# Optimization experiments

Hardware: AMD Instinct MI355X
Metric: run time of the kernel (lower is better)

The kernel has to match this reference:

```python
import jax, jax.numpy as jnp
import numpy as np

EPS = 1e-7  # Keras K.epsilon()
ROUTINGS = 3

def squash(v, axis=-1):
    s2 = jnp.sum(jnp.square(v), axis=axis, keepdims=True)
    scale = s2 / (1.0 + s2) / jnp.sqrt(s2 + EPS)
    return scale * v

def setup_inputs() -> dict:
    key = jax.random.key(0)
    k1, k2 = jax.random.split(key)
    inputs = jax.random.normal(k1, (64, 1152, 8), dtype=jnp.float32)
    W = jax.random.normal(k2, (8, 43, 16), dtype=jnp.float32) * 0.1  # glorot-ish scale
    return {"inputs": inputs, "W": W}

def reference(inputs, W):
    # inputs: [b, i, j] (batch, input_num_capsule, input_dim_capsule)
    # W: [j, k, l] -> inputs_hat: [b, i, k, l]
    inputs_hat = jnp.einsum('bij,jkl->bikl', inputs, W)
    b_sz, I, N, _ = inputs_hat.shape
    b = jnp.zeros((b_sz, I, N), dtype=inputs_hat.dtype)
    outputs = None
    for r in range(ROUTINGS):
        c = jax.nn.softmax(b, axis=2)                       # [b, i, k]
        s = jnp.einsum('bik,bikl->bkl', c, inputs_hat)      # [b, k, l]
        outputs = squash(s, axis=-1)                         # [b, k, l]
        if r < ROUTINGS - 1:
            agreement = jnp.einsum('bikl,bkl->bik', inputs_hat, outputs)
            b = b + agreement
    return outputs
```

## Files before the change

kernel.cpp:

```cpp
#include <hip/hip_runtime.h>

#define EPS 1e-7f
#define NB 64
#define NI 1152
#define NJ 8
#define NK 43
#define NL 16
#define KL (NK*NL)
#define NSLICE 8
#define SLICE 144
#define THREADS 384
#define NKG 11
#define CPS 148
#define PARTS 344
#define WVSZ 352
#define SVP 17

__device__ __forceinline__ void load_slice(int tid, const float* __restrict__ Xb, int sl,
                                           float4* sXa, float4* sXb) {
    if (tid < SLICE*2) {
        const float4* Xs4 = (const float4*)(Xb + (size_t)sl*SLICE*NJ);
        float4 v = Xs4[tid];
        if (tid & 1) sXb[tid >> 1] = v; else sXa[tid >> 1] = v;
    }
}

__device__ __forceinline__ float squash_scale(float sv) {
    float sq = sv * sv;
    sq += __shfl_xor(sq, 1);
    sq += __shfl_xor(sq, 2);
    sq += __shfl_xor(sq, 4);
    sq += __shfl_xor(sq, 8);
    const float scale = sq / ((1.f + sq) * sqrtf(sq + EPS));
    return scale * sv;
}

template<bool ATOMIC>
__device__ __forceinline__ void routing_main(
    int tid, const float4* sXa, const float4* sXb,
    const float (*sWv)[44], float4* cP, float* __restrict__ gpOut)
{
    if (tid < SLICE) {
        float4 x0 = sXa[tid], x1 = sXb[tid];
        float xr[NJ] = {x0.x, x0.y, x0.z, x0.w, x1.x, x1.y, x1.z, x1.w};
        float a[44];
        #pragma unroll
        for (int k = 0; k < 44; ++k) a[k] = 0.f;
        #pragma unroll
        for (int j = 0; j < NJ; ++j) {
            #pragma unroll
            for (int k4 = 0; k4 < NKG; ++k4) {
                float4 wv = *(const float4*)&sWv[j][k4*4];
                a[k4*4+0] = fmaf(xr[j], wv.x, a[k4*4+0]);
                a[k4*4+1] = fmaf(xr[j], wv.y, a[k4*4+1]);
                a[k4*4+2] = fmaf(xr[j], wv.z, a[k4*4+2]);
                a[k4*4+3] = fmaf(xr[j], wv.w, a[k4*4+3]);
            }
        }
        float m0=a[0], m1=a[1], m2=a[2], m3=a[3];
        #pragma unroll
        for (int k = 4; k < 40; k += 4) {
            m0 = fmaxf(m0, a[k+0]); m1 = fmaxf(m1, a[k+1]);
            m2 = fmaxf(m2, a[k+2]); m3 = fmaxf(m3, a[k+3]);
        }
        m0 = fmaxf(m0, a[40]); m1 = fmaxf(m1, a[41]); m2 = fmaxf(m2, a[42]);
        const float m = fmaxf(fmaxf(m0, m1), fmaxf(m2, m3));
        float z0=0.f, z1=0.f, z2=0.f, z3=0.f;
        #pragma unroll
        for (int k = 0; k < 40; k += 4) {
            a[k+0] = __expf(a[k+0]-m); z0 += a[k+0];
            a[k+1] = __expf(a[k+1]-m); z1 += a[k+1];
            a[k+2] = __expf(a[k+2]-m); z2 += a[k+2];
            a[k+3] = __expf(a[k+3]-m); z3 += a[k+3];
        }
        a[40] = __expf(a[40]-m); z0 += a[40];
        a[41] = __expf(a[41]-m); z1 += a[41];
        a[42] = __expf(a[42]-m); z2 += a[42];
        const float inv = 1.f / ((z0+z1) + (z2+z3));
        #pragma unroll
        for (int k = 0; k < NK; ++k) a[k] *= inv;
        a[43] = 0.f;
        #pragma unroll
        for (int kg = 0; kg < NKG; ++kg)
            cP[kg*CPS + tid] = make_float4(a[4*kg], a[4*kg+1], a[4*kg+2], a[4*kg+3]);
    }
    __syncthreads();
    if (tid < NKG*16) {
        const int kg = tid >> 4, s = tid & 15;
        float acc[4][8];
        #pragma unroll
        for (int q = 0; q < 4; ++q)
            #pragma unroll
            for (int j = 0; j < 8; ++j) acc[q][j] = 0.f;
        #pragma unroll
        for (int ii = 0; ii < SLICE/16; ++ii) {
            const int il = s + 16*ii;
            float4 c4 = cP[kg*CPS + il];
            float4 xa = sXa[il], xb = sXb[il];
            acc[0][0]=fmaf(c4.x,xa.x,acc[0][0]); acc[0][1]=fmaf(c4.x,xa.y,acc[0][1]);
            acc[0][2]=fmaf(c4.x,xa.z,acc[0][2]); acc[0][3]=fmaf(c4.x,xa.w,acc[0][3]);
            acc[0][4]=fmaf(c4.x,xb.x,acc[0][4]); acc[0][5]=fmaf(c4.x,xb.y,acc[0][5]);
            acc[0][6]=fmaf(c4.x,xb.z,acc[0][6]); acc[0][7]=fmaf(c4.x,xb.w,acc[0][7]);
            acc[1][0]=fmaf(c4.y,xa.x,acc[1][0]); acc[1][1]=fmaf(c4.y,xa.y,acc[1][1]);
            acc[1][2]=fmaf(c4.y,xa.z,acc[1][2]); acc[1][3]=fmaf(c4.y,xa.w,acc[1][3]);
            acc[1][4]=fmaf(c4.y,xb.x,acc[1][4]); acc[1][5]=fmaf(c4.y,xb.y,acc[1][5]);
            acc[1][6]=fmaf(c4.y,xb.z,acc[1][6]); acc[1][7]=fmaf(c4.y,xb.w,acc[1][7]);
            acc[2][0]=fmaf(c4.z,xa.x,acc[2][0]); acc[2][1]=fmaf(c4.z,xa.y,acc[2][1]);
            acc[2][2]=fmaf(c4.z,xa.z,acc[2][2]); acc[2][3]=fmaf(c4.z,xa.w,acc[2][3]);
            acc[2][4]=fmaf(c4.z,xb.x,acc[2][4]); acc[2][5]=fmaf(c4.z,xb.y,acc[2][5]);
            acc[2][6]=fmaf(c4.z,xb.z,acc[2][6]); acc[2][7]=fmaf(c4.z,xb.w,acc[2][7]);
            acc[3][0]=fmaf(c4.w,xa.x,acc[3][0]); acc[3][1]=fmaf(c4.w,xa.y,acc[3][1]);
            acc[3][2]=fmaf(c4.w,xa.z,acc[3][2]); acc[3][3]=fmaf(c4.w,xa.w,acc[3][3]);
            acc[3][4]=fmaf(c4.w,xb.x,acc[3][4]); acc[3][5]=fmaf(c4.w,xb.y,acc[3][5]);
            acc[3][6]=fmaf(c4.w,xb.z,acc[3][6]); acc[3][7]=fmaf(c4.w,xb.w,acc[3][7]);
        }
        float cur[32];
        #pragma unroll
        for (int q = 0; q < 4; ++q)
            #pragma unroll
            for (int j = 0; j < 8; ++j) cur[q*8+j] = acc[q][j];
        {   const bool up = (tid & 8) != 0;
            #pragma unroll
            for (int v = 0; v < 16; ++v) {
                float give = up ? cur[v] : cur[v+16];
                float keep = up ? cur[v+16] : cur[v];
                cur[v] = keep + __shfl_xor(give, 8);
            } }
        {   const bool up = (tid & 4) != 0;
            #pragma unroll
            for (int v = 0; v < 8; ++v) {
                float give = up ? cur[v] : cur[v+8];
                float keep = up ? cur[v+8] : cur[v];
                cur[v] = keep + __shfl_xor(give, 4);
            } }
        {   const bool up = (tid & 2) != 0;
            #pragma unroll
            for (int v = 0; v < 4; ++v) {
                float give = up ? cur[v] : cur[v+4];
                float keep = up ? cur[v+4] : cur[v];
                cur[v] = keep + __shfl_xor(give, 2);
            } }
        {   const bool up = (tid & 1) != 0;
            #pragma unroll
            for (int v = 0; v < 2; ++v) {
                float give = up ? cur[v] : cur[v+2];
                float keep = up ? cur[v+2] : cur[v];
                cur[v] = keep + __shfl_xor(give, 1);
            } }
        const int p = kg*32 + (s << 1);
        if (p < PARTS) {
            if (ATOMIC) {
                __hip_atomic_store(&gpOut[p],   cur[0], __ATOMIC_RELAXED, __HIP_MEMORY_SCOPE_AGENT);
                __hip_atomic_store(&gpOut[p+1], cur[1], __ATOMIC_RELAXED, __HIP_MEMORY_SCOPE_AGENT);
            } else {
                *(float2*)&gpOut[p] = make_float2(cur[0], cur[1]);
            }
        }
    }
}

__global__ __launch_bounds__(THREADS, 3)
void caps_k1(const float* __restrict__ X, const float* __restrict__ W,
             float* __restrict__ wv0g, float* __restrict__ gp1,
             int* __restrict__ cnt) {
    __shared__ __align__(16) float4 sXa[SLICE], sXb[SLICE];
    __shared__ __align__(16) float4 cP[NKG*CPS];
    __shared__ __align__(16) float sWv[NJ][44];
    __shared__ __align__(16) float sV[NK*SVP];
    __shared__ __align__(16) float4 xsW[12];
    __shared__ float sXs[NJ];

    const int tid = threadIdx.x;
    const int b  = blockIdx.x >> 3;
    const int sl = blockIdx.x & 7;
    const float* Xb = X + (size_t)b * (NI*NJ);

    if (sl == 0 && tid == 0) cnt[b] = 0;

    load_slice(tid, Xb, sl, sXa, sXb);
    {
        const float4* X4 = (const float4*)Xb;
        float4 ax = X4[tid];
        #pragma unroll
        for (int r = 1; r < 6; ++r) {
            float4 v = X4[tid + r*THREADS];
            ax.x += v.x; ax.y += v.y; ax.z += v.z; ax.w += v.w;
        }
        #pragma unroll
        for (int msk = 2; msk <= 32; msk <<= 1) {
            ax.x += __shfl_xor(ax.x, msk);
            ax.y += __shfl_xor(ax.y, msk);
            ax.z += __shfl_xor(ax.z, msk);
            ax.w += __shfl_xor(ax.w, msk);
        }
        if ((tid & 63) < 2) xsW[(tid >> 6)*2 + (tid & 1)] = ax;
    }
    __syncthreads();
    if (tid < NJ) {
        const float* f = (const float*)xsW;
        float s = 0.f;
        #pragma unroll
        for (int w = 0; w < 6; ++w) s += f[(w*2 + (tid >> 2))*4 + (tid & 3)];
        sXs[tid] = s;
    }
    __syncthreads();
    for (int t = tid; t < KL; t += THREADS) {
        float sv = 0.f;
        #pragma unroll
        for (int j = 0; j < NJ; ++j) sv = fmaf(sXs[j], W[j*KL + t], sv);
        sv *= (1.0f/43.0f);
        sV[(t >> 4)*SVP + (t & 15)] = squash_scale(sv);
    }
    __syncthreads();
    if (tid < WVSZ) {
        const int j = tid / 44, k = tid % 44;
        float wv = 0.f;
        if (k < NK) {
            #pragma unroll
            for (int l = 0; l < NL; ++l)
                wv = fmaf(W[j*KL + k*NL + l], sV[k*SVP + l], wv);
        }
        ((float*)sWv)[tid] = wv;
        if (sl == 0) wv0g[(size_t)b*WVSZ + tid] = wv;
    }
    __syncthreads();
    routing_main<false>(tid, sXa, sXb, sWv, cP, gp1 + (size_t)(b*NSLICE + sl)*PARTS);
}

__global__ __launch_bounds__(THREADS, 3)
void caps_k2(const float* __restrict__ X, const float* __restrict__ W,
             const float* __restrict__ wv0g, const float* __restrict__ gp1,
             float* __restrict__ gp2, int* __restrict__ cnt,
             float* __restrict__ out) {
    __shared__ __align__(16) float4 sXa[SLICE], sXb[SLICE];
    __shared__ __align__(16) float4 cP[NKG*CPS];
    __shared__ __align__(16) float sWv[NJ][44];
    __shared__ __align__(16) float sV[NK*SVP];
    __shared__ float sG[PARTS];
    __shared__ int sLast;

    const int tid = threadIdx.x;
    const int b  = blockIdx.x >> 3;
    const int sl = blockIdx.x & 7;
    const float* Xb = X + (size_t)b * (NI*NJ);

    load_slice(tid, Xb, sl, sXa, sXb);
    if (tid < PARTS) {
        float g = 0.f;
        #pragma unroll
        for (int q = 0; q < NSLICE; ++q) g += gp1[(size_t)(b*NSLICE + q)*PARTS + tid];
        sG[tid] = g;
    }
    __syncthreads();
    for (int t = tid; t < KL; t += THREADS) {
        const int k8 = (t >> 4)*8;
        float sv = 0.f;
        #pragma unroll
        for (int j = 0; j < NJ; ++j) sv = fmaf(sG[k8 + j], W[j*KL + t], sv);
        sV[(t >> 4)*SVP + (t & 15)] = squash_scale(sv);
    }
    __syncthreads();
    if (tid < WVSZ) {
        const int j = tid / 44, k = tid % 44;
        float wv = 0.f;
        if (k < NK) {
            #pragma unroll
            for (int l = 0; l < NL; ++l)
                wv = fmaf(W[j*KL + k*NL + l], sV[k*SVP + l], wv);
        }
        ((float*)sWv)[tid] = wv0g[(size_t)b*WVSZ + tid] + wv;
    }
    __syncthreads();
    routing_main<true>(tid, sXa, sXb, sWv, cP, gp2 + (size_t)(b*NSLICE + sl)*PARTS);

    asm volatile("s_waitcnt vmcnt(0)" ::: "memory");
    __syncthreads();
    if (tid == 0) {
        int old = __hip_atomic_fetch_add(&cnt[b], 1, __ATOMIC_RELAXED, __HIP_MEMORY_SCOPE_AGENT);
        sLast = (old == NSLICE - 1) ? 1 : 0;
    }
    __syncthreads();
    if (!sLast) return;
    if (tid < PARTS) {
        float g = 0.f;
        #pragma unroll
        for (int q = 0; q < NSLICE; ++q)
            g += __hip_atomic_load(&gp2[(size_t)(b*NSLICE + q)*PARTS + tid],
                                   __ATOMIC_RELAXED, __HIP_MEMORY_SCOPE_AGENT);
        sG[tid] = g;
    }
    __syncthreads();
    for (int t = tid; t < KL; t += THREADS) {
        const int k8 = (t >> 4)*8;
        float sv = 0.f;
        #pragma unroll
        for (int j = 0; j < NJ; ++j) sv = fmaf(sG[k8 + j], W[j*KL + t], sv);
        out[(size_t)b*KL + t] = squash_scale(sv);
    }
}

extern "C" void kernel_launch(void* const* d_in, const int* in_sizes, int n_in,
                              void* d_out, int out_size, void* d_ws, size_t ws_size,
                              hipStream_t stream) {
    const float* X = (const float*)d_in[0];
    const float* W = (const float*)d_in[1];
    float* out = (float*)d_out;
    float* wv0 = (float*)d_ws;
    float* gp1 = wv0 + NB*WVSZ;
    float* gp2 = gp1 + NB*NSLICE*PARTS;
    int*   cnt = (int*)(gp2 + NB*NSLICE*PARTS);
    hipLaunchKernelGGL(caps_k1, dim3(NB*NSLICE), dim3(THREADS), 0, stream, X, W, wv0, gp1, cnt);
    hipLaunchKernelGGL(caps_k2, dim3(NB*NSLICE), dim3(THREADS), 0, stream, X, W, wv0, gp1, gp2, cnt, out);
}
```

Baseline: 26.24 us.

## Fuse two routing kernels into one with per-batch spin barrier

Merges the two launches into a single kernel. The eight slice blocks of each batch now meet at a global atomic counter with a spin-wait barrier, and the first-iteration weight vector stays in shared memory instead of going through a workspace round trip. The counters are cleared by a memset before the launch. This removes one kernel launch and one global write and read. The cost is spin-waiting, which relies on all 512 blocks being co-resident (3 blocks per CU at 384 threads), and an extra memset call in the stream.

```diff
diff --git a/kernel.cpp b/kernel.cpp
--- a/kernel.cpp
+++ b/kernel.cpp
@@ -15,15 +15,7 @@
 #define PARTS 344
 #define WVSZ 352
 #define SVP 17
-
-__device__ __forceinline__ void load_slice(int tid, const float* __restrict__ Xb, int sl,
-                                           float4* sXa, float4* sXb) {
-    if (tid < SLICE*2) {
-        const float4* Xs4 = (const float4*)(Xb + (size_t)sl*SLICE*NJ);
-        float4 v = Xs4[tid];
-        if (tid & 1) sXb[tid >> 1] = v; else sXa[tid >> 1] = v;
-    }
-}
+#define SPIN_LIMIT 200000000u
 
 __device__ __forceinline__ float squash_scale(float sv) {
     float sq = sv * sv;
@@ -35,10 +27,9 @@
     return scale * sv;
 }
 
-template<bool ATOMIC>
 __device__ __forceinline__ void routing_main(
     int tid, const float4* sXa, const float4* sXb,
-    const float (*sWv)[44], float4* cP, float* __restrict__ gpOut)
+    const float* sWv, float4* cP, float* __restrict__ gpOut)
 {
     if (tid < SLICE) {
         float4 x0 = sXa[tid], x1 = sXb[tid];
@@ -50,7 +41,7 @@
         for (int j = 0; j < NJ; ++j) {
             #pragma unroll
             for (int k4 = 0; k4 < NKG; ++k4) {
-                float4 wv = *(const float4*)&sWv[j][k4*4];
+                float4 wv = *(const float4*)&sWv[j*44 + k4*4];
                 a[k4*4+0] = fmaf(xr[j], wv.x, a[k4*4+0]);
                 a[k4*4+1] = fmaf(xr[j], wv.y, a[k4*4+1]);
                 a[k4*4+2] = fmaf(xr[j], wv.z, a[k4*4+2]);
@@ -149,35 +140,36 @@
             } }
         const int p = kg*32 + (s << 1);
         if (p < PARTS) {
-            if (ATOMIC) {
-                __hip_atomic_store(&gpOut[p],   cur[0], __ATOMIC_RELAXED, __HIP_MEMORY_SCOPE_AGENT);
-                __hip_atomic_store(&gpOut[p+1], cur[1], __ATOMIC_RELAXED, __HIP_MEMORY_SCOPE_AGENT);
-            } else {
-                *(float2*)&gpOut[p] = make_float2(cur[0], cur[1]);
-            }
+            __hip_atomic_store(&gpOut[p],   cur[0], __ATOMIC_RELAXED, __HIP_MEMORY_SCOPE_AGENT);
+            __hip_atomic_store(&gpOut[p+1], cur[1], __ATOMIC_RELAXED, __HIP_MEMORY_SCOPE_AGENT);
         }
     }
 }
 
 __global__ __launch_bounds__(THREADS, 3)
-void caps_k1(const float* __restrict__ X, const float* __restrict__ W,
-             float* __restrict__ wv0g, float* __restrict__ gp1,
-             int* __restrict__ cnt) {
+void caps_all(const float* __restrict__ X, const float* __restrict__ W,
+              float* __restrict__ gp1, float* __restrict__ gp2,
+              int* __restrict__ cnt1, int* __restrict__ cnt2,
+              float* __restrict__ out) {
     __shared__ __align__(16) float4 sXa[SLICE], sXb[SLICE];
     __shared__ __align__(16) float4 cP[NKG*CPS];
-    __shared__ __align__(16) float sWv[NJ][44];
+    __shared__ __align__(16) float sWv[WVSZ];
     __shared__ __align__(16) float sV[NK*SVP];
+    __shared__ float sG[PARTS];
     __shared__ __align__(16) float4 xsW[12];
     __shared__ float sXs[NJ];
+    __shared__ int sLast;
 
     const int tid = threadIdx.x;
     const int b  = blockIdx.x >> 3;
     const int sl = blockIdx.x & 7;
     const float* Xb = X + (size_t)b * (NI*NJ);
 
-    if (sl == 0 && tid == 0) cnt[b] = 0;
-
-    load_slice(tid, Xb, sl, sXa, sXb);
+    if (tid < SLICE*2) {
+        const float4* Xs4 = (const float4*)(Xb + (size_t)sl*SLICE*NJ);
+        float4 v = Xs4[tid];
+        if (tid & 1) sXb[tid >> 1] = v; else sXa[tid >> 1] = v;
+    }
     {
         const float4* X4 = (const float4*)Xb;
         float4 ax = X4[tid];
@@ -220,35 +212,28 @@
             for (int l = 0; l < NL; ++l)
                 wv = fmaf(W[j*KL + k*NL + l], sV[k*SVP + l], wv);
         }
-        ((float*)sWv)[tid] = wv;
-        if (sl == 0) wv0g[(size_t)b*WVSZ + tid] = wv;
-    }
-    __syncthreads();
-    routing_main<false>(tid, sXa, sXb, sWv, cP, gp1 + (size_t)(b*NSLICE + sl)*PARTS);
-}
-
-__global__ __launch_bounds__(THREADS, 3)
-void caps_k2(const float* __restrict__ X, const float* __restrict__ W,
-             const float* __restrict__ wv0g, const float* __restrict__ gp1,
-             float* __restrict__ gp2, int* __restrict__ cnt,
-             float* __restrict__ out) {
-    __shared__ __align__(16) float4 sXa[SLICE], sXb[SLICE];
-    __shared__ __align__(16) float4 cP[NKG*CPS];
-    __shared__ __align__(16) float sWv[NJ][44];
-    __shared__ __align__(16) float sV[NK*SVP];
-    __shared__ float sG[PARTS];
-    __shared__ int sLast;
-
-    const int tid = threadIdx.x;
-    const int b  = blockIdx.x >> 3;
-    const int sl = blockIdx.x & 7;
-    const float* Xb = X + (size_t)b * (NI*NJ);
-
-    load_slice(tid, Xb, sl, sXa, sXb);
+        sWv[tid] = wv;
+    }
+    __syncthreads();
+
+    routing_main(tid, sXa, sXb, sWv, cP, gp1 + (size_t)(b*NSLICE + sl)*PARTS);
+
+    asm volatile("s_waitcnt vmcnt(0)" ::: "memory");
+    __syncthreads();
+    if (tid == 0) {
+        __hip_atomic_fetch_add(&cnt1[b], 1, __ATOMIC_RELAXED, __HIP_MEMORY_SCOPE_AGENT);
+        unsigned spins = 0;
+        while (__hip_atomic_load(&cnt1[b], __ATOMIC_RELAXED, __HIP_MEMORY_SCOPE_AGENT) < NSLICE
+               && ++spins < SPIN_LIMIT)
+            __builtin_amdgcn_s_sleep(1);
+    }
+    __syncthreads();
     if (tid < PARTS) {
         float g = 0.f;
         #pragma unroll
-        for (int q = 0; q < NSLICE; ++q) g += gp1[(size_t)(b*NSLICE + q)*PARTS + tid];
+        for (int q = 0; q < NSLICE; ++q)
+            g += __hip_atomic_load(&gp1[(size_t)(b*NSLICE + q)*PARTS + tid],
+                                   __ATOMIC_RELAXED, __HIP_MEMORY_SCOPE_AGENT);
         sG[tid] = g;
     }
     __syncthreads();
@@ -268,15 +253,16 @@
             for (int l = 0; l < NL; ++l)
                 wv = fmaf(W[j*KL + k*NL + l], sV[k*SVP + l], wv);
         }
-        ((float*)sWv)[tid] = wv0g[(size_t)b*WVSZ + tid] + wv;
-    }
-    __syncthreads();
-    routing_main<true>(tid, sXa, sXb, sWv, cP, gp2 + (size_t)(b*NSLICE + sl)*PARTS);
+        sWv[tid] += wv;
+    }
+    __syncthreads();
+
+    routing_main(tid, sXa, sXb, sWv, cP, gp2 + (size_t)(b*NSLICE + sl)*PARTS);
 
     asm volatile("s_waitcnt vmcnt(0)" ::: "memory");
     __syncthreads();
     if (tid == 0) {
-        int old = __hip_atomic_fetch_add(&cnt[b], 1, __ATOMIC_RELAXED, __HIP_MEMORY_SCOPE_AGENT);
+        int old = __hip_atomic_fetch_add(&cnt2[b], 1, __ATOMIC_RELAXED, __HIP_MEMORY_SCOPE_AGENT);
         sLast = (old == NSLICE - 1) ? 1 : 0;
     }
     __syncthreads();
@@ -305,10 +291,10 @@
     const float* X = (const float*)d_in[0];
     const float* W = (const float*)d_in[1];
     float* out = (float*)d_out;
-    float* wv0 = (float*)d_ws;
-    float* gp1 = wv0 + NB*WVSZ;
+    float* gp1 = (float*)d_ws;
     float* gp2 = gp1 + NB*NSLICE*PARTS;
     int*   cnt = (int*)(gp2 + NB*NSLICE*PARTS);
-    hipLaunchKernelGGL(caps_k1, dim3(NB*NSLICE), dim3(THREADS), 0, stream, X, W, wv0, gp1, cnt);
-    hipLaunchKernelGGL(caps_k2, dim3(NB*NSLICE), dim3(THREADS), 0, stream, X, W, wv0, gp1, gp2, cnt, out);
+    hipMemsetAsync(cnt, 0, 2*NB*sizeof(int), stream);
+    hipLaunchKernelGGL(caps_all, dim3(NB*NSLICE), dim3(THREADS), 0, stream,
+                       X, W, gp1, gp2, cnt, cnt + NB, out);
 }
```

Result: slower. 34.96 us (+33.2%).
